# Kernel optimization log

Hardware: AMD Instinct MI355X
Metric: run time of the kernel (lower is better)

Reference implementation:

```python
import jax, jax.numpy as jnp
import numpy as np

B, D, ADA, INTER, RANK = 16, 2048, 1024, 1024, 8

def setup_inputs() -> dict:
    key = jax.random.key(0)
    ks = jax.random.split(key, 7)
    s = lambda fan_in: 1.0 / np.sqrt(fan_in)
    return {
        "x": jax.random.normal(ks[0], (B, D), jnp.float32),
        "ada_emb": jax.random.normal(ks[1], (B, ADA), jnp.float32),
        "base": jax.random.normal(ks[2], (D, D), jnp.float32),  # nn.Parameter(torch.randn)
        "w1": jax.random.normal(ks[3], (ADA, INTER), jnp.float32) * s(ADA),
        "b1": jax.random.normal(ks[4], (INTER,), jnp.float32) * s(ADA),
        "w2": jax.random.normal(ks[5], (INTER, D * RANK * 2), jnp.float32) * s(INTER),
        "b2": jax.random.normal(ks[6], (D * RANK * 2,), jnp.float32) * s(INTER),
    }

def reference(x, ada_emb, base, w1, b1, w2, b2):
    Bn, Dn = x.shape
    # gen_weight: Linear -> GELU (exact, erf-based as torch nn.GELU) -> Linear
    h = jax.nn.gelu(ada_emb @ w1 + b1, approximate=False)
    xw = h @ w2 + b2                               # [B, D*rank*2]
    x_a, x_b = jnp.split(xw, 2, axis=-1)
    r = x_a.shape[-1] // Dn
    x_a = x_a.reshape(Bn, Dn, r)                   # [B, D, r]
    x_b = x_b.reshape(Bn, Dn, r)                   # [B, D, r]
    # per-sample low-rank delta + base: layer[b,d,k] = base[d,k] + sum_r x_a[b,d,r]*x_b[b,k,r]
    layer = base[None, :, :] + jnp.einsum('bdr,bkr->bdk', x_a, x_b)  # [B, D, D]
    out = jnp.einsum('bc,bco->bo', x, layer)       # batched matvec
    return x + out                                 # residual
```

## Files before the change

kernel.cpp:

```cpp
#include <hip/hip_runtime.h>
#include <math.h>

#define BN 16
#define DN 2048
#define ADA 1024
#define INTER 1024
#define NW2 32768
#define HALFN 16384
#define KSL 16

typedef __attribute__((address_space(1))) const void gv_t;
typedef __attribute__((address_space(3))) void lv_t;
__device__ __forceinline__ void gload_lds16(const float* g, float* l) {
    __builtin_amdgcn_global_load_lds((gv_t*)g, (lv_t*)l, 16, 0, 0);
}
#define WAITV4() asm volatile("s_waitcnt vmcnt(4)" ::: "memory")
#define WAITV0() asm volatile("s_waitcnt vmcnt(0)" ::: "memory")
#define WAITL0() asm volatile("s_waitcnt lgkmcnt(0)" ::: "memory")

__global__ void k1a(const float* __restrict__ ada, const float* __restrict__ w1,
                    float* __restrict__ h_pre) {
    const int j  = blockIdx.x * 256 + threadIdx.x;
    const int k0 = blockIdx.y * 32;
    __shared__ float a_lds[BN][32];
    for (int idx = threadIdx.x; idx < BN * 32; idx += 256) {
        int m = idx >> 5, kk = idx & 31;
        a_lds[m][kk] = ada[m * ADA + k0 + kk];
    }
    __syncthreads();
    float acc[BN];
#pragma unroll
    for (int m = 0; m < BN; ++m) acc[m] = 0.f;
    for (int kk = 0; kk < 32; ++kk) {
        float w = w1[(k0 + kk) * INTER + j];
#pragma unroll
        for (int m = 0; m < BN; ++m) acc[m] += a_lds[m][kk] * w;
    }
#pragma unroll
    for (int m = 0; m < BN; ++m) atomicAdd(&h_pre[m * INTER + j], acc[m]);
}

__global__ void k1bt(const float* __restrict__ h_pre, const float* __restrict__ b1,
                     float* __restrict__ h_t) {
    int i = blockIdx.x * 256 + threadIdx.x;
    int m = i >> 10, j = i & (INTER - 1);
    float v = h_pre[i] + b1[j];
    float g = 0.5f * v * (1.f + erff(v * 0.70710678118654752f));
    h_t[j * BN + m] = g;
}

__global__ __launch_bounds__(256) void k2p(const float* __restrict__ h_t,
                                           const float* __restrict__ w2,
                                           float* __restrict__ p2) {
    const int tid = threadIdx.x;
    const int wv  = tid >> 6, ln = tid & 63;
    const int n0  = blockIdx.x * 1024;
    const int k0  = blockIdx.y * 64;
    __shared__ __align__(16) float wl[3][4][1024];
    __shared__ __align__(16) float hl[64][16];

    ((float4*)hl)[tid] = ((const float4*)(h_t + k0 * BN))[tid];
    WAITL0();

    float4 acc[BN];
#pragma unroll
    for (int m = 0; m < BN; ++m) acc[m] = make_float4(0.f, 0.f, 0.f, 0.f);

#define STAGE(b, ph) do {                                                     \
    const float* gs_ = w2 + (size_t)(k0 + (ph) * 4) * NW2 + n0                \
                     + wv * 256 + ln * 4;                                     \
    float* ls_ = &wl[b][0][wv * 256];                                         \
    gload_lds16(gs_ + (size_t)0 * NW2, ls_ + 0 * 1024);                       \
    gload_lds16(gs_ + (size_t)1 * NW2, ls_ + 1 * 1024);                       \
    gload_lds16(gs_ + (size_t)2 * NW2, ls_ + 2 * 1024);                       \
    gload_lds16(gs_ + (size_t)3 * NW2, ls_ + 3 * 1024);                       \
} while (0)
#define AC(m, hs) do { acc[m].x = fmaf(hs, wvv.x, acc[m].x);                  \
                       acc[m].y = fmaf(hs, wvv.y, acc[m].y);                  \
                       acc[m].z = fmaf(hs, wvv.z, acc[m].z);                  \
                       acc[m].w = fmaf(hs, wvv.w, acc[m].w); } while (0)
#define COMPUTE(b, ph) do {                                                   \
    _Pragma("unroll")                                                         \
    for (int i_ = 0; i_ < 4; ++i_) {                                          \
        const int kk_ = (ph) * 4 + i_;                                        \
        const float4 wvv = ((const float4*)&wl[b][i_][0])[tid];               \
        const float4 h0 = ((const float4*)&hl[kk_][0])[0];                    \
        const float4 h1 = ((const float4*)&hl[kk_][0])[1];                    \
        const float4 h2 = ((const float4*)&hl[kk_][0])[2];                    \
        const float4 h3 = ((const float4*)&hl[kk_][0])[3];                    \
        AC(0,  h0.x); AC(1,  h0.y); AC(2,  h0.z); AC(3,  h0.w);               \
        AC(4,  h1.x); AC(5,  h1.y); AC(6,  h1.z); AC(7,  h1.w);               \
        AC(8,  h2.x); AC(9,  h2.y); AC(10, h2.z); AC(11, h2.w);               \
        AC(12, h3.x); AC(13, h3.y); AC(14, h3.z); AC(15, h3.w);               \
    }                                                                         \
} while (0)

    STAGE(0, 0);
    STAGE(1, 1);
    int cb = 0, nb = 2;
    for (int ph = 0; ph < 15; ++ph) {
        WAITV4();
        __builtin_amdgcn_s_barrier();
        if (ph < 14) STAGE(nb, ph + 2);
        COMPUTE(cb, ph);
        cb = (cb == 2) ? 0 : cb + 1;
        nb = (nb == 2) ? 0 : nb + 1;
    }
    WAITV0();
    __builtin_amdgcn_s_barrier();
    COMPUTE(cb, 15);
#undef COMPUTE
#undef AC
#undef STAGE

    float* op = p2 + (size_t)blockIdx.y * (BN * NW2) + n0 + tid * 4;
#pragma unroll
    for (int m = 0; m < BN; ++m)
        *(float4*)(op + (size_t)m * NW2) = acc[m];
}

__global__ void k2r(const float* __restrict__ p2, const float* __restrict__ b2,
                    float* __restrict__ xw) {
    const int i  = blockIdx.x * 256 + threadIdx.x;
    const int n4 = i & (NW2 / 4 - 1);
    float4 s = ((const float4*)b2)[n4];
    const float4* p = (const float4*)p2 + i;
#pragma unroll
    for (int ks = 0; ks < KSL; ++ks) {
        float4 v = p[(size_t)ks * (BN * NW2 / 4)];
        s.x += v.x; s.y += v.y; s.z += v.z; s.w += v.w;
    }
    ((float4*)xw)[i] = s;
}

__global__ void k3(const float* __restrict__ x, const float* __restrict__ xw,
                   float* __restrict__ t) {
    const int m = blockIdx.x >> 3, r = blockIdx.x & 7;
    float s = 0.f;
    for (int c = threadIdx.x; c < DN; c += 256)
        s += x[m * DN + c] * xw[(size_t)m * NW2 + c * 8 + r];
    __shared__ float red[256];
    red[threadIdx.x] = s;
    __syncthreads();
    for (int off = 128; off > 0; off >>= 1) {
        if (threadIdx.x < off) red[threadIdx.x] += red[threadIdx.x + off];
        __syncthreads();
    }
    if (threadIdx.x == 0) t[m * 8 + r] = red[0];
}

#define K4ACC(i, xv) do { acc[i].x = fmaf((xv), b.x, acc[i].x); \
                          acc[i].y = fmaf((xv), b.y, acc[i].y); \
                          acc[i].z = fmaf((xv), b.z, acc[i].z); \
                          acc[i].w = fmaf((xv), b.w, acc[i].w); } while (0)
__global__ __launch_bounds__(256) void k4m(const float* __restrict__ x,
                                           const float* __restrict__ base,
                                           float* __restrict__ p4) {
    const int o4 = blockIdx.x * 256 + threadIdx.x;
    const int c0 = blockIdx.y * 32;
    const int m0 = blockIdx.z * 8;
    float4 acc[8];
#pragma unroll
    for (int m = 0; m < 8; ++m) acc[m] = make_float4(0.f, 0.f, 0.f, 0.f);

    const float4* bp = (const float4*)base + (size_t)c0 * (DN / 4) + o4;
    float4 bbuf[8];
#pragma unroll
    for (int u = 0; u < 8; ++u) bbuf[u] = bp[(size_t)u * (DN / 4)];

    for (int cb = 0; cb < 32; cb += 8) {
#pragma unroll
        for (int u = 0; u < 8; ++u) {
            const int cc = cb + u;
            const float4 b = bbuf[u];
            const int cn = (cc + 8 < 32) ? (cc + 8) : cc;
            bbuf[u] = bp[(size_t)cn * (DN / 4)];
            const float x0 = x[(m0 + 0) * DN + c0 + cc];
            const float x1 = x[(m0 + 1) * DN + c0 + cc];
            const float x2 = x[(m0 + 2) * DN + c0 + cc];
            const float x3 = x[(m0 + 3) * DN + c0 + cc];
            const float x4 = x[(m0 + 4) * DN + c0 + cc];
            const float x5 = x[(m0 + 5) * DN + c0 + cc];
            const float x6 = x[(m0 + 6) * DN + c0 + cc];
            const float x7 = x[(m0 + 7) * DN + c0 + cc];
            K4ACC(0, x0); K4ACC(1, x1); K4ACC(2, x2); K4ACC(3, x3);
            K4ACC(4, x4); K4ACC(5, x5); K4ACC(6, x6); K4ACC(7, x7);
        }
    }
    float4* op = (float4*)p4 + (size_t)blockIdx.y * (BN * DN / 4)
               + (size_t)m0 * (DN / 4) + o4;
#pragma unroll
    for (int m = 0; m < 8; ++m) op[(size_t)m * (DN / 4)] = acc[m];
}

__global__ void k5(const float* __restrict__ x, const float* __restrict__ p4,
                   const float* __restrict__ xw, const float* __restrict__ t,
                   float* __restrict__ out) {
    const int i = blockIdx.x * 256 + threadIdx.x;
    const int m = i >> 11, o = i & (DN - 1);
    float s = x[i];
    const float* p = p4 + i;
#pragma unroll 8
    for (int ks = 0; ks < 64; ++ks) s += p[ks * (BN * DN)];
    const float4 xb0 = *(const float4*)(xw + (size_t)m * NW2 + HALFN + o * 8);
    const float4 xb1 = *(const float4*)(xw + (size_t)m * NW2 + HALFN + o * 8 + 4);
    const float* tm = t + m * 8;
    s += tm[0] * xb0.x + tm[1] * xb0.y + tm[2] * xb0.z + tm[3] * xb0.w
       + tm[4] * xb1.x + tm[5] * xb1.y + tm[6] * xb1.z + tm[7] * xb1.w;
    out[i] = s;
}

extern "C" void kernel_launch(void* const* d_in, const int* in_sizes, int n_in,
                              void* d_out, int out_size, void* d_ws, size_t ws_size,
                              hipStream_t stream) {
    const float* x    = (const float*)d_in[0];
    const float* ada  = (const float*)d_in[1];
    const float* base = (const float*)d_in[2];
    const float* w1   = (const float*)d_in[3];
    const float* b1   = (const float*)d_in[4];
    const float* w2   = (const float*)d_in[5];
    const float* b2   = (const float*)d_in[6];
    float* out = (float*)d_out;
    char* ws = (char*)d_ws;

    float* p2    = (float*)(ws);
    float* xw    = (float*)(ws + 33554432);
    float* p4    = (float*)(ws + 35651584);
    float* h_pre = (float*)(ws + 44040192);
    float* h_t   = (float*)(ws + 44105728);
    float* t     = (float*)(ws + 44171264);

    hipMemsetAsync(h_pre, 0, 65536, stream);

    k1a <<<dim3(4, 32),    256, 0, stream>>>(ada, w1, h_pre);
    k1bt<<<64,             256, 0, stream>>>(h_pre, b1, h_t);
    k2p <<<dim3(32, KSL),  256, 0, stream>>>(h_t, w2, p2);
    k4m <<<dim3(2, 64, 2), 256, 0, stream>>>(x, base, p4);
    k2r <<<512,            256, 0, stream>>>(p2, b2, xw);
    k3  <<<128,            256, 0, stream>>>(x, xw, t);
    k5  <<<128,            256, 0, stream>>>(x, p4, xw, t, out);
}
```

Before: 72.54 us.

## Use per-wave LDS buffers in w2 GEMM to drop barriers; fuse t reduction into k2r

The w2 streaming GEMM now gives each wave its own 4-deep LDS ring, so each wave only reads data it loaded itself. This removes the block-wide barriers between pipeline stages and keeps three stages in flight instead of two. Separately, the x_a dot-product reduction (old k3) is folded into the split-K reduction kernel using an LDS tree reduction and atomics, which removes one launch and one re-read of xw. The costs are more LDS per block and atomic accumulation into t, which is zeroed by an enlarged memset.

```diff
diff --git a/kernel.cpp b/kernel.cpp
--- a/kernel.cpp
+++ b/kernel.cpp
@@ -14,9 +14,9 @@
 __device__ __forceinline__ void gload_lds16(const float* g, float* l) {
     __builtin_amdgcn_global_load_lds((gv_t*)g, (lv_t*)l, 16, 0, 0);
 }
+#define WAITV8() asm volatile("s_waitcnt vmcnt(8)" ::: "memory")
 #define WAITV4() asm volatile("s_waitcnt vmcnt(4)" ::: "memory")
 #define WAITV0() asm volatile("s_waitcnt vmcnt(0)" ::: "memory")
-#define WAITL0() asm volatile("s_waitcnt lgkmcnt(0)" ::: "memory")
 
 __global__ void k1a(const float* __restrict__ ada, const float* __restrict__ w1,
                     float* __restrict__ h_pre) {
@@ -49,18 +49,18 @@
     h_t[j * BN + m] = g;
 }
 
-__global__ __launch_bounds__(256) void k2p(const float* __restrict__ h_t,
+__global__ __launch_bounds__(256) void k2w(const float* __restrict__ h_t,
                                            const float* __restrict__ w2,
                                            float* __restrict__ p2) {
     const int tid = threadIdx.x;
     const int wv  = tid >> 6, ln = tid & 63;
     const int n0  = blockIdx.x * 1024;
     const int k0  = blockIdx.y * 64;
-    __shared__ __align__(16) float wl[3][4][1024];
+    __shared__ __align__(16) float wl[4][4][1024];
     __shared__ __align__(16) float hl[64][16];
 
     ((float4*)hl)[tid] = ((const float4*)(h_t + k0 * BN))[tid];
-    WAITL0();
+    __syncthreads();
 
     float4 acc[BN];
 #pragma unroll
@@ -69,11 +69,11 @@
 #define STAGE(b, ph) do {                                                     \
     const float* gs_ = w2 + (size_t)(k0 + (ph) * 4) * NW2 + n0                \
                      + wv * 256 + ln * 4;                                     \
-    float* ls_ = &wl[b][0][wv * 256];                                         \
-    gload_lds16(gs_ + (size_t)0 * NW2, ls_ + 0 * 1024);                       \
-    gload_lds16(gs_ + (size_t)1 * NW2, ls_ + 1 * 1024);                       \
-    gload_lds16(gs_ + (size_t)2 * NW2, ls_ + 2 * 1024);                       \
-    gload_lds16(gs_ + (size_t)3 * NW2, ls_ + 3 * 1024);                       \
+    float* ls_ = &wl[wv][b][0];                                               \
+    gload_lds16(gs_ + (size_t)0 * NW2, ls_ + 0);                              \
+    gload_lds16(gs_ + (size_t)1 * NW2, ls_ + 256);                            \
+    gload_lds16(gs_ + (size_t)2 * NW2, ls_ + 512);                            \
+    gload_lds16(gs_ + (size_t)3 * NW2, ls_ + 768);                            \
 } while (0)
 #define AC(m, hs) do { acc[m].x = fmaf(hs, wvv.x, acc[m].x);                  \
                        acc[m].y = fmaf(hs, wvv.y, acc[m].y);                  \
@@ -83,7 +83,7 @@
     _Pragma("unroll")                                                         \
     for (int i_ = 0; i_ < 4; ++i_) {                                          \
         const int kk_ = (ph) * 4 + i_;                                        \
-        const float4 wvv = ((const float4*)&wl[b][i_][0])[tid];               \
+        const float4 wvv = *(const float4*)&wl[wv][b][i_ * 256 + ln * 4];     \
         const float4 h0 = ((const float4*)&hl[kk_][0])[0];                    \
         const float4 h1 = ((const float4*)&hl[kk_][0])[1];                    \
         const float4 h2 = ((const float4*)&hl[kk_][0])[2];                    \
@@ -97,33 +97,35 @@
 
     STAGE(0, 0);
     STAGE(1, 1);
-    int cb = 0, nb = 2;
-    for (int ph = 0; ph < 15; ++ph) {
-        WAITV4();
-        __builtin_amdgcn_s_barrier();
-        if (ph < 14) STAGE(nb, ph + 2);
-        COMPUTE(cb, ph);
-        cb = (cb == 2) ? 0 : cb + 1;
-        nb = (nb == 2) ? 0 : nb + 1;
-    }
+    STAGE(2, 2);
+#pragma unroll 1
+    for (int ph = 0; ph <= 13; ++ph) {
+        WAITV8();
+        if (ph <= 12) STAGE((ph + 3) & 3, ph + 3);
+        COMPUTE(ph & 3, ph);
+    }
+    WAITV4();
+    COMPUTE(14 & 3, 14);
     WAITV0();
-    __builtin_amdgcn_s_barrier();
-    COMPUTE(cb, 15);
+    COMPUTE(15 & 3, 15);
 #undef COMPUTE
 #undef AC
 #undef STAGE
 
-    float* op = p2 + (size_t)blockIdx.y * (BN * NW2) + n0 + tid * 4;
+    float* op = p2 + (size_t)blockIdx.y * (BN * NW2) + n0 + wv * 256 + ln * 4;
 #pragma unroll
     for (int m = 0; m < BN; ++m)
         *(float4*)(op + (size_t)m * NW2) = acc[m];
 }
 
 __global__ void k2r(const float* __restrict__ p2, const float* __restrict__ b2,
-                    float* __restrict__ xw) {
-    const int i  = blockIdx.x * 256 + threadIdx.x;
-    const int n4 = i & (NW2 / 4 - 1);
-    float4 s = ((const float4*)b2)[n4];
+                    const float* __restrict__ x, float* __restrict__ xw,
+                    float* __restrict__ t) {
+    const int tid = threadIdx.x;
+    const int i   = blockIdx.x * 256 + tid;
+    const int m   = i >> 13;
+    const int f4  = i & 8191;
+    float4 s = ((const float4*)b2)[f4];
     const float4* p = (const float4*)p2 + i;
 #pragma unroll
     for (int ks = 0; ks < KSL; ++ks) {
@@ -131,22 +133,28 @@
         s.x += v.x; s.y += v.y; s.z += v.z; s.w += v.w;
     }
     ((float4*)xw)[i] = s;
-}
-
-__global__ void k3(const float* __restrict__ x, const float* __restrict__ xw,
-                   float* __restrict__ t) {
-    const int m = blockIdx.x >> 3, r = blockIdx.x & 7;
-    float s = 0.f;
-    for (int c = threadIdx.x; c < DN; c += 256)
-        s += x[m * DN + c] * xw[(size_t)m * NW2 + c * 8 + r];
-    __shared__ float red[256];
-    red[threadIdx.x] = s;
-    __syncthreads();
-    for (int off = 128; off > 0; off >>= 1) {
-        if (threadIdx.x < off) red[threadIdx.x] += red[threadIdx.x + off];
-        __syncthreads();
-    }
-    if (threadIdx.x == 0) t[m * 8 + r] = red[0];
+
+    const bool is_xa = (f4 < 4096);
+    if (is_xa) {
+        __shared__ float4 lr[256];
+        const int c = f4 >> 1;
+        const float xv = x[m * DN + c];
+        lr[tid] = make_float4(s.x * xv, s.y * xv, s.z * xv, s.w * xv);
+        for (int off = 128; off >= 2; off >>= 1) {
+            __syncthreads();
+            if (tid < off) {
+                float4 a = lr[tid], b = lr[tid + off];
+                lr[tid] = make_float4(a.x + b.x, a.y + b.y, a.z + b.z, a.w + b.w);
+            }
+        }
+        if (tid == 0) {
+            atomicAdd(&t[m * 8 + 0], lr[0].x); atomicAdd(&t[m * 8 + 1], lr[0].y);
+            atomicAdd(&t[m * 8 + 2], lr[0].z); atomicAdd(&t[m * 8 + 3], lr[0].w);
+        } else if (tid == 1) {
+            atomicAdd(&t[m * 8 + 4], lr[1].x); atomicAdd(&t[m * 8 + 5], lr[1].y);
+            atomicAdd(&t[m * 8 + 6], lr[1].z); atomicAdd(&t[m * 8 + 7], lr[1].w);
+        }
+    }
 }
 
 #define K4ACC(i, xv) do { acc[i].x = fmaf((xv), b.x, acc[i].x); \
@@ -227,16 +235,15 @@
     float* xw    = (float*)(ws + 33554432);
     float* p4    = (float*)(ws + 35651584);
     float* h_pre = (float*)(ws + 44040192);
-    float* h_t   = (float*)(ws + 44105728);
-    float* t     = (float*)(ws + 44171264);
-
-    hipMemsetAsync(h_pre, 0, 65536, stream);
+    float* t     = (float*)(ws + 44105728);
+    float* h_t   = (float*)(ws + 44106240);
+
+    hipMemsetAsync(h_pre, 0, 66048, stream);
 
     k1a <<<dim3(4, 32),    256, 0, stream>>>(ada, w1, h_pre);
     k1bt<<<64,             256, 0, stream>>>(h_pre, b1, h_t);
-    k2p <<<dim3(32, KSL),  256, 0, stream>>>(h_t, w2, p2);
+    k2w <<<dim3(32, KSL),  256, 0, stream>>>(h_t, w2, p2);
     k4m <<<dim3(2, 64, 2), 256, 0, stream>>>(x, base, p4);
-    k2r <<<512,            256, 0, stream>>>(p2, b2, xw);
-    k3  <<<128,            256, 0, stream>>>(x, xw, t);
+    k2r <<<512,            256, 0, stream>>>(p2, b2, x, xw, t);
     k5  <<<128,            256, 0, stream>>>(x, p4, xw, t, out);
 }
```

After: 76.25 us. 5.1% more time.
